# Optimization experiments

Measured on AMD Instinct MI355X. Metric: run time of the kernel, lower is better.

## Reference

```python
import jax, jax.numpy as jnp
import numpy as np

N, E, G, S = 200000, 800000, 2048, 128
NUM_OPS, NUM_ETYPES, NUMERIC = 64, 4, 12
H, TEXT, VOCAB, OUT = 256, 64, 30000, 512
IN0 = 32 + NUMERIC  # 44


def _ln(h, eps=1e-5):
    # nn.LayerNorm with default (ones/zeros) affine, created fresh each forward
    m = h.mean(-1, keepdims=True)
    v = ((h - m) ** 2).mean(-1, keepdims=True)
    return (h - m) * jax.lax.rsqrt(v + eps)


def _leaky(v):
    return jnp.where(v > 0, v, 0.1 * v)  # LeakyReLU(0.1)


def setup_inputs() -> dict:
    key = jax.random.key(0)
    ks = jax.random.split(key, 40)
    x = jax.random.normal(ks[0], (N, 1 + NUMERIC), jnp.float32)
    x = x.at[:, 0].set(jax.random.randint(ks[1], (N,), 0, NUM_OPS).astype(jnp.float32))
    inp = {
        'x': x,
        'edge_index': jax.random.randint(ks[2], (2, E), 0, N),
        'edge_attr': jax.random.randint(ks[3], (E,), 0, NUM_ETYPES),
        'batch': jnp.sort(jax.random.randint(ks[4], (N,), 0, G)),
        'sql_ids': jax.random.randint(ks[5], (G, S), 0, VOCAB),
        'sql_mask': (jax.random.uniform(ks[6], (G, S)) > 0.3).astype(jnp.float32),
        'op_embed': jax.random.normal(ks[7], (NUM_OPS, 32), jnp.float32),
        'edge_embed': jax.random.normal(ks[8], (NUM_ETYPES, 16), jnp.float32),
        'token_embed': jax.random.normal(ks[9], (VOCAB, TEXT), jnp.float32).at[0].set(0.0),  # padding_idx=0
    }
    dims = [IN0, H, H]
    k = 10
    for i, d in enumerate(dims):
        inp[f'lin_w{i}'] = jax.random.normal(ks[k], (d, 16), jnp.float32) * 0.05; k += 1
        inp[f'lin_b{i}'] = jnp.zeros((d,), jnp.float32)
        inp[f'eps{i}'] = jnp.zeros((), jnp.float32)  # train_eps init 0
        inp[f'W1_{i}'] = jax.random.normal(ks[k], (H, d), jnp.float32) * 0.05; k += 1
        inp[f'b1_{i}'] = jnp.zeros((H,), jnp.float32)
        inp[f'W2_{i}'] = jax.random.normal(ks[k], (H, H), jnp.float32) * 0.05; k += 1
        inp[f'b2_{i}'] = jnp.zeros((H,), jnp.float32)
    inp['mW1'] = jax.random.normal(ks[k], (H, H + 3 + TEXT), jnp.float32) * 0.05; k += 1
    inp['mb1'] = jnp.zeros((H,), jnp.float32)
    inp['mW2'] = jax.random.normal(ks[k], (OUT, H), jnp.float32) * 0.05
    inp['mb2'] = jnp.zeros((OUT,), jnp.float32)
    return inp


def reference(x, edge_index, edge_attr, batch, sql_ids, sql_mask,
              op_embed, edge_embed, token_embed,
              lin_w0, lin_b0, eps0, W1_0, b1_0, W2_0, b2_0,
              lin_w1, lin_b1, eps1, W1_1, b1_1, W2_1, b2_1,
              lin_w2, lin_b2, eps2, W1_2, b1_2, W2_2, b2_2,
              mW1, mb1, mW2, mb2):
    op_ids = jnp.clip(x[:, 0].astype(jnp.int32), 0, NUM_OPS - 1)
    nums = x[:, 1:]
    e_idx = jnp.minimum(edge_attr, NUM_ETYPES - 1)  # clamp_max
    edge_emb = edge_embed[e_idx]                    # [E,16]
    h = jnp.concatenate([op_embed[op_ids], nums], 1)  # [N,44]
    src, dst = edge_index[0], edge_index[1]
    convs = [(lin_w0, lin_b0, eps0, W1_0, b1_0, W2_0, b2_0),
             (lin_w1, lin_b1, eps1, W1_1, b1_1, W2_1, b2_1),
             (lin_w2, lin_b2, eps2, W1_2, b1_2, W2_2, b2_2)]
    for (lw, lb, eps, W1, b1, W2, b2) in convs:
        h_in = h
        # GINEConv: msg = relu(x_j + Lin(edge_attr)); sum-aggregate at dst
        msg = jax.nn.relu(h[src] + edge_emb @ lw.T + lb)        # [E,d]
        aggr = jax.ops.segment_sum(msg, dst, num_segments=h.shape[0])
        z = (1.0 + eps) * h + aggr
        h = jax.nn.relu(z @ W1.T + b1) @ W2.T + b2              # conv MLP -> [N,H]
        h = _ln(h)
        h = _leaky(h + h_in) if h_in.shape[-1] == h.shape[-1] else _leaky(h)
    # graph pooling
    g = jax.ops.segment_sum(h, batch, num_segments=G)            # global_add_pool
    count = jax.ops.segment_sum(jnp.ones((h.shape[0],), h.dtype), batch, num_segments=G)
    denom = jnp.maximum(count, 1.0)                              # scatter_mean semantics
    fanout_mean = jax.ops.segment_sum(x[:, 5], batch, num_segments=G) / denom
    cost_mean = jax.ops.segment_sum(x[:, 4], batch, num_segments=G) / denom
    graph_sum = jnp.stack([count, fanout_mean, cost_mean], 1)    # [G,3]
    # text pooling (masked mean)
    emb = token_embed[sql_ids]                                   # [G,S,TEXT]
    summed = (emb * sql_mask[..., None]).sum(1)
    lengths = jnp.maximum(sql_mask.sum(1, keepdims=True), 1.0)
    text_feat = summed / lengths
    cat = jnp.concatenate([g, graph_sum, text_feat], 1)          # [G, H+3+TEXT]
    hid = _leaky(cat @ mW1.T + mb1)                              # Dropout(0.1) is identity in eval
    return hid @ mW2.T + mb2                                     # [G, OUT]
```

## Files before the change

### kernel.cpp

```cpp
#include <hip/hip_runtime.h>

#define NN 200000
#define EE 800000
#define GG 2048
#define NBLK ((NN + 255) / 256)

typedef __attribute__((ext_vector_type(8))) short short8;
typedef __attribute__((ext_vector_type(4))) float f32x4;

__device__ __forceinline__ float bf2f(ushort u){
  unsigned x = ((unsigned)u) << 16;
  return __uint_as_float(x);
}
__device__ __forceinline__ ushort f2bf(float f){
  unsigned x = __float_as_uint(f);
  x += 0x7fffu + ((x >> 16) & 1u);
  return (ushort)(x >> 16);
}

__device__ __forceinline__ void swz256(const float* __restrict__ W, ushort* __restrict__ o, int idx){
  int ks = idx >> 13, rem = idx & 8191;
  int j16 = rem >> 9, rem2 = rem & 511;
  int ln = rem2 >> 3, t = rem2 & 7;
  int row = j16*16 + (ln & 15);
  int k = ks*32 + (ln >> 4)*8 + t;
  o[idx] = f2bf(W[(size_t)row*256 + k]);
}

__global__ __launch_bounds__(256) void prep_k(
    const float* __restrict__ W10, const float* __restrict__ W20,
    const float* __restrict__ W11, const float* __restrict__ W21,
    const float* __restrict__ W12, const float* __restrict__ W22,
    const float* __restrict__ lw0, const float* __restrict__ lb0,
    const float* __restrict__ lw1, const float* __restrict__ lb1,
    const float* __restrict__ lw2, const float* __restrict__ lb2,
    const float* __restrict__ eE, const float* __restrict__ mW1,
    const float* __restrict__ mW2,
    ushort* __restrict__ wb10, ushort* __restrict__ wb20,
    ushort* __restrict__ wb11, ushort* __restrict__ wb21,
    ushort* __restrict__ wb12, ushort* __restrict__ wb22,
    ushort* __restrict__ mW1b, ushort* __restrict__ mW2b,
    float* __restrict__ eb)
{
  int b = blockIdx.x, tid = threadIdx.x;
  if (b < 64){
    int idx = b*256 + tid;
    int ks = idx >> 13, rem = idx & 8191;
    int j16 = rem >> 9, rem2 = rem & 511;
    int ln = rem2 >> 3, t = rem2 & 7;
    int row = j16*16 + (ln & 15);
    int k = ks*32 + (ln >> 4)*8 + t;
    wb10[idx] = (k < 44) ? f2bf(W10[row*44 + k]) : (ushort)0;
    return;
  }
  b -= 64;
  if (b < 256){ swz256(W20, wb20, b*256+tid); return; } b -= 256;
  if (b < 256){ swz256(W11, wb11, b*256+tid); return; } b -= 256;
  if (b < 256){ swz256(W21, wb21, b*256+tid); return; } b -= 256;
  if (b < 256){ swz256(W12, wb12, b*256+tid); return; } b -= 256;
  if (b < 256){ swz256(W22, wb22, b*256+tid); return; } b -= 256;
  if (b < 384){
    int idx = b*256 + tid; int o = idx / 384, k = idx - o*384;
    mW1b[idx] = (k < 323) ? f2bf(mW1[(size_t)o*323 + k]) : (ushort)0;
    return;
  }
  b -= 384;
  if (b < 512){ int idx = b*256+tid; mW2b[idx] = f2bf(mW2[idx]); return; } b -= 512;
  int li = b >> 2, t = b & 3;
  const float* lw = (li == 0) ? lw0 : ((li == 1) ? lw1 : lw2);
  const float* lb = (li == 0) ? lb0 : ((li == 1) ? lb1 : lb2);
  int d = (li == 0) ? 44 : 256;
  float v = 0.f;
  if (tid < d){
    float a = 0.f;
    #pragma unroll
    for (int j = 0; j < 16; j++) a += eE[t*16 + j] * lw[tid*16 + j];
    v = a + lb[tid];
  }
  eb[(li*4 + t)*256 + tid] = v;
}

__global__ __launch_bounds__(256) void build_h0_k(
    const float* __restrict__ x, const float* __restrict__ opE, ushort* __restrict__ h0)
{
  int idx = blockIdx.x*256 + threadIdx.x;
  int i = idx >> 6, c = idx & 63;
  float v = 0.f;
  if (c < 32){
    int op = (int)x[(size_t)i*13];
    op = op < 0 ? 0 : (op > 63 ? 63 : op);
    v = opE[op*32 + c];
  } else if (c < 44){
    v = x[(size_t)i*13 + (c - 31)];
  }
  h0[idx] = f2bf(v);
}

__global__ __launch_bounds__(256) void deg_k(const int* __restrict__ dst, int* __restrict__ D){
  int e = blockIdx.x*256 + threadIdx.x;
  atomicAdd(&D[dst[e]], 1);
}
__global__ __launch_bounds__(256) void scan1_k(int* __restrict__ D, int* __restrict__ bsum){
  __shared__ int s[256];
  int b = blockIdx.x, t = threadIdx.x, idx = b*256 + t;
  int v = (idx < NN) ? D[idx] : 0;
  s[t] = v; __syncthreads();
  for (int off = 1; off < 256; off <<= 1){
    int u = (t >= off) ? s[t-off] : 0;
    __syncthreads();
    s[t] += u;
    __syncthreads();
  }
  if (idx < NN) D[idx] = s[t] - v;
  if (t == 255) bsum[b] = s[255];
}
__global__ __launch_bounds__(256) void scan2_k(int* __restrict__ bsum){
  __shared__ int s[256];
  __shared__ int carry;
  int t = threadIdx.x;
  if (t == 0) carry = 0;
  __syncthreads();
  for (int c0 = 0; c0 < NBLK; c0 += 256){
    int idx = c0 + t;
    int v = (idx < NBLK) ? bsum[idx] : 0;
    s[t] = v; __syncthreads();
    for (int off = 1; off < 256; off <<= 1){
      int u = (t >= off) ? s[t-off] : 0;
      __syncthreads();
      s[t] += u;
      __syncthreads();
    }
    int ex = s[t] - v + carry;
    if (idx < NBLK) bsum[idx] = ex;
    int tot = s[255];
    __syncthreads();
    if (t == 0) carry += tot;
    __syncthreads();
  }
}
__global__ __launch_bounds__(256) void scan3_k(int* __restrict__ D, const int* __restrict__ bsum){
  int b = blockIdx.x, idx = b*256 + threadIdx.x;
  if (idx < NN) D[idx] += bsum[b];
}
__global__ __launch_bounds__(256) void fill_k(const int* __restrict__ src, const int* __restrict__ dst,
                                              const int* __restrict__ et, int* __restrict__ D,
                                              int* __restrict__ csr){
  int e = blockIdx.x*256 + threadIdx.x;
  int d = dst[e];
  int t = et[e]; t = t < 3 ? t : 3;
  int pos = atomicAdd(&D[d], 1);
  csr[pos] = src[e] | (t << 18);
}

template<int KD, int RESID>
__global__ __launch_bounds__(256) void layerf_k(
    const ushort* __restrict__ hsrc, const int* __restrict__ Dend, const int* __restrict__ csr,
    const float* __restrict__ ebL,
    const ushort* __restrict__ W1s, const float* __restrict__ b1,
    const ushort* __restrict__ W2s, const float* __restrict__ b2,
    const float* __restrict__ epsp, ushort* __restrict__ hout)
{
  __shared__ ushort ZT[32][264];
  __shared__ float ebs[1024];
  __shared__ float red1[32][4], red2[32][4], mnL[32], rsL[32];
  const int tid = threadIdx.x, lane = tid & 63, wv = tid >> 6;
  const int l15 = lane & 15, lq = lane >> 4;
  const int rowBase = blockIdx.x * 32;
  const float epv = 1.0f + epsp[0];
  const char* hb = (const char*)hsrc;

  if (KD == 256){
    for (int i = tid; i < 1024; i += 256) ebs[i] = ebL[i];
  } else {
    if (tid < 256) ebs[tid] = ebL[(tid >> 6)*256 + (tid & 63)];
  }
  __syncthreads();

  if (KD == 256){
    const int c = lane * 4;
    const unsigned c2 = lane * 8;
    #pragma unroll 1
    for (int it = 0; it < 2; it++){
      int rr0 = wv*8 + it*4;
      int r0 = rowBase + rr0;
      float4 A0, A1, A2, A3;
      {
        ushort4 q0 = *(const ushort4*)(hb + (size_t)(r0+0)*512 + c2);
        ushort4 q1 = *(const ushort4*)(hb + (size_t)(r0+1)*512 + c2);
        ushort4 q2 = *(const ushort4*)(hb + (size_t)(r0+2)*512 + c2);
        ushort4 q3 = *(const ushort4*)(hb + (size_t)(r0+3)*512 + c2);
        A0 = make_float4(epv*bf2f(q0.x), epv*bf2f(q0.y), epv*bf2f(q0.z), epv*bf2f(q0.w));
        A1 = make_float4(epv*bf2f(q1.x), epv*bf2f(q1.y), epv*bf2f(q1.z), epv*bf2f(q1.w));
        A2 = make_float4(epv*bf2f(q2.x), epv*bf2f(q2.y), epv*bf2f(q2.z), epv*bf2f(q2.w));
        A3 = make_float4(epv*bf2f(q3.x), epv*bf2f(q3.y), epv*bf2f(q3.z), epv*bf2f(q3.w));
      }
      int bm1 = (r0 == 0) ? 0 : Dend[r0-1];
      int e0 = Dend[r0], e1 = Dend[r0+1], e2 = Dend[r0+2], e3 = Dend[r0+3];
      int st0 = bm1, st1 = e0, st2 = e1, st3 = e2;
      int n0 = e0 - st0, n1 = e1 - st1, n2 = e2 - st2, n3 = e3 - st3;
      int nmax = n0 > n1 ? n0 : n1;
      nmax = nmax > n2 ? nmax : n2;
      nmax = nmax > n3 ? nmax : n3;
      ushort4 z4; z4.x = z4.y = z4.z = z4.w = 0;
      ushort4 sv0 = z4, sv1 = z4, sv2 = z4, sv3 = z4;
      int t0 = 0, t1 = 0, t2 = 0, t3 = 0;
      if (n0 > 0){ int p = csr[st0]; sv0 = *(const ushort4*)(hb + (unsigned)((p & 0x3FFFF) << 9) + c2); t0 = ((p >> 18) & 3)*256; }
      if (n1 > 0){ int p = csr[st1]; sv1 = *(const ushort4*)(hb + (unsigned)((p & 0x3FFFF) << 9) + c2); t1 = ((p >> 18) & 3)*256; }
      if (n2 > 0){ int p = csr[st2]; sv2 = *(const ushort4*)(hb + (unsigned)((p & 0x3FFFF) << 9) + c2); t2 = ((p >> 18) & 3)*256; }
      if (n3 > 0){ int p = csr[st3]; sv3 = *(const ushort4*)(hb + (unsigned)((p & 0x3FFFF) << 9) + c2); t3 = ((p >> 18) & 3)*256; }
      for (int k = 0; k < nmax; k++){
        ushort4 c0 = sv0, c1 = sv1, c2v = sv2, c3 = sv3;
        int u0 = t0, u1 = t1, u2 = t2, u3 = t3;
        if (k+1 < n0){ int p = csr[st0+k+1]; sv0 = *(const ushort4*)(hb + (unsigned)((p & 0x3FFFF) << 9) + c2); t0 = ((p >> 18) & 3)*256; }
        if (k+1 < n1){ int p = csr[st1+k+1]; sv1 = *(const ushort4*)(hb + (unsigned)((p & 0x3FFFF) << 9) + c2); t1 = ((p >> 18) & 3)*256; }
        if (k+1 < n2){ int p = csr[st2+k+1]; sv2 = *(const ushort4*)(hb + (unsigned)((p & 0x3FFFF) << 9) + c2); t2 = ((p >> 18) & 3)*256; }
        if (k+1 < n3){ int p = csr[st3+k+1]; sv3 = *(const ushort4*)(hb + (unsigned)((p & 0x3FFFF) << 9) + c2); t3 = ((p >> 18) & 3)*256; }
        if (k < n0){
          const float4 ev = *(const float4*)&ebs[u0 + c];
          float v;
          v = bf2f(c0.x) + ev.x; A0.x += v > 0.f ? v : 0.f;
          v = bf2f(c0.y) + ev.y; A0.y += v > 0.f ? v : 0.f;
          v = bf2f(c0.z) + ev.z; A0.z += v > 0.f ? v : 0.f;
          v = bf2f(c0.w) + ev.w; A0.w += v > 0.f ? v : 0.f;
        }
        if (k < n1){
          const float4 ev = *(const float4*)&ebs[u1 + c];
          float v;
          v = bf2f(c1.x) + ev.x; A1.x += v > 0.f ? v : 0.f;
          v = bf2f(c1.y) + ev.y; A1.y += v > 0.f ? v : 0.f;
          v = bf2f(c1.z) + ev.z; A1.z += v > 0.f ? v : 0.f;
          v = bf2f(c1.w) + ev.w; A1.w += v > 0.f ? v : 0.f;
        }
        if (k < n2){
          const float4 ev = *(const float4*)&ebs[u2 + c];
          float v;
          v = bf2f(c2v.x) + ev.x; A2.x += v > 0.f ? v : 0.f;
          v = bf2f(c2v.y) + ev.y; A2.y += v > 0.f ? v : 0.f;
          v = bf2f(c2v.z) + ev.z; A2.z += v > 0.f ? v : 0.f;
          v = bf2f(c2v.w) + ev.w; A2.w += v > 0.f ? v : 0.f;
        }
        if (k < n3){
          const float4 ev = *(const float4*)&ebs[u3 + c];
          float v;
          v = bf2f(c3.x) + ev.x; A3.x += v > 0.f ? v : 0.f;
          v = bf2f(c3.y) + ev.y; A3.y += v > 0.f ? v : 0.f;
          v = bf2f(c3.z) + ev.z; A3.z += v > 0.f ? v : 0.f;
          v = bf2f(c3.w) + ev.w; A3.w += v > 0.f ? v : 0.f;
        }
      }
      ushort4 o;
      o.x = f2bf(A0.x); o.y = f2bf(A0.y); o.z = f2bf(A0.z); o.w = f2bf(A0.w);
      *(ushort4*)&ZT[rr0+0][c] = o;
      o.x = f2bf(A1.x); o.y = f2bf(A1.y); o.z = f2bf(A1.z); o.w = f2bf(A1.w);
      *(ushort4*)&ZT[rr0+1][c] = o;
      o.x = f2bf(A2.x); o.y = f2bf(A2.y); o.z = f2bf(A2.z); o.w = f2bf(A2.w);
      *(ushort4*)&ZT[rr0+2][c] = o;
      o.x = f2bf(A3.x); o.y = f2bf(A3.y); o.z = f2bf(A3.z); o.w = f2bf(A3.w);
      *(ushort4*)&ZT[rr0+3][c] = o;
    }
  } else {
    const int c = l15 * 4;
    const unsigned c2 = l15 * 8;
    #pragma unroll 1
    for (int it = 0; it < 2; it++){
      int rr = wv*8 + it*4 + lq;
      int r = rowBase + rr;
      const ushort4 hv = *(const ushort4*)(hb + (size_t)r*128 + c2);
      float a0 = epv*bf2f(hv.x), a1 = epv*bf2f(hv.y), a2 = epv*bf2f(hv.z), a3 = epv*bf2f(hv.w);
      int st = (r == 0) ? 0 : Dend[r-1];
      int en = Dend[r];
      if (st < en){
        int p = csr[st];
        ushort4 sv = *(const ushort4*)(hb + (unsigned)((p & 0x3FFFF) << 7) + c2);
        int tt = ((p >> 18) & 3)*64;
        for (int e = st; e < en; e++){
          ushort4 cur = sv; int tc = tt;
          int e2 = (e+1 < en) ? e+1 : e;
          int p2 = csr[e2];
          sv = *(const ushort4*)(hb + (unsigned)((p2 & 0x3FFFF) << 7) + c2);
          tt = ((p2 >> 18) & 3)*64;
          const float4 ev = *(const float4*)&ebs[tc + c];
          float v;
          v = bf2f(cur.x) + ev.x; a0 += v > 0.f ? v : 0.f;
          v = bf2f(cur.y) + ev.y; a1 += v > 0.f ? v : 0.f;
          v = bf2f(cur.z) + ev.z; a2 += v > 0.f ? v : 0.f;
          v = bf2f(cur.w) + ev.w; a3 += v > 0.f ? v : 0.f;
        }
      }
      ushort4 o; o.x=f2bf(a0); o.y=f2bf(a1); o.z=f2bf(a2); o.w=f2bf(a3);
      *(ushort4*)&ZT[rr][c] = o;
    }
  }
  __syncthreads();

  f32x4 acc[2][4];
  #pragma unroll
  for (int i = 0; i < 2; i++)
    #pragma unroll
    for (int j = 0; j < 4; j++){ f32x4 z = {0.f,0.f,0.f,0.f}; acc[i][j] = z; }

  #pragma unroll
  for (int s = 0; s < KD/32; s++){
    short8 af[2], bfv[4];
    #pragma unroll
    for (int j = 0; j < 4; j++)
      bfv[j] = *(const short8*)(W1s + ((size_t)(s*16 + wv*4 + j)*64 + lane)*8);
    #pragma unroll
    for (int i = 0; i < 2; i++)
      af[i] = *(const short8*)&ZT[i*16 + l15][s*32 + lq*8];
    #pragma unroll
    for (int i = 0; i < 2; i++)
      #pragma unroll
      for (int j = 0; j < 4; j++)
        acc[i][j] = __builtin_amdgcn_mfma_f32_16x16x32_bf16(af[i], bfv[j], acc[i][j], 0, 0, 0);
  }
  __syncthreads();

  {
    float b1c[4];
    #pragma unroll
    for (int j = 0; j < 4; j++) b1c[j] = b1[wv*64 + j*16 + l15];
    #pragma unroll
    for (int i = 0; i < 2; i++)
      #pragma unroll
      for (int j = 0; j < 4; j++){
        int cc = wv*64 + j*16 + l15;
        #pragma unroll
        for (int rg = 0; rg < 4; rg++){
          int r = i*16 + (lq << 2) + rg;
          float v = acc[i][j][rg] + b1c[j];
          v = v > 0.f ? v : 0.f;
          ZT[r][cc] = f2bf(v);
        }
      }
  }
  __syncthreads();

  #pragma unroll
  for (int i = 0; i < 2; i++)
    #pragma unroll
    for (int j = 0; j < 4; j++){ f32x4 z = {0.f,0.f,0.f,0.f}; acc[i][j] = z; }

  #pragma unroll
  for (int s = 0; s < 8; s++){
    short8 af[2], bfv[4];
    #pragma unroll
    for (int j = 0; j < 4; j++)
      bfv[j] = *(const short8*)(W2s + ((size_t)(s*16 + wv*4 + j)*64 + lane)*8);
    #pragma unroll
    for (int i = 0; i < 2; i++)
      af[i] = *(const short8*)&ZT[i*16 + l15][s*32 + lq*8];
    #pragma unroll
    for (int i = 0; i < 2; i++)
      #pragma unroll
      for (int j = 0; j < 4; j++)
        acc[i][j] = __builtin_amdgcn_mfma_f32_16x16x32_bf16(af[i], bfv[j], acc[i][j], 0, 0, 0);
  }

  float b2c[4];
  #pragma unroll
  for (int j = 0; j < 4; j++) b2c[j] = b2[wv*64 + j*16 + l15];
  #pragma unroll
  for (int i = 0; i < 2; i++){
    #pragma unroll
    for (int rg = 0; rg < 4; rg++){
      float s1 = 0.f, s2 = 0.f;
      #pragma unroll
      for (int j = 0; j < 4; j++){
        float y = acc[i][j][rg] + b2c[j];
        s1 += y; s2 += y*y;
      }
      #pragma unroll
      for (int m = 1; m < 16; m <<= 1){
        s1 += __shfl_xor(s1, m, 64);
        s2 += __shfl_xor(s2, m, 64);
      }
      if (l15 == 0){
        int r = i*16 + (lq << 2) + rg;
        red1[r][wv] = s1; red2[r][wv] = s2;
      }
    }
  }
  __syncthreads();
  if (tid < 32){
    float s1 = red1[tid][0] + red1[tid][1] + red1[tid][2] + red1[tid][3];
    float s2 = red2[tid][0] + red2[tid][1] + red2[tid][2] + red2[tid][3];
    float mn = s1 * (1.f/256.f);
    float vr = s2 * (1.f/256.f) - mn*mn;
    mnL[tid] = mn;
    rsL[tid] = rsqrtf(vr + 1e-5f);
  }
  __syncthreads();
  #pragma unroll
  for (int i = 0; i < 2; i++){
    #pragma unroll
    for (int rg = 0; rg < 4; rg++){
      int r = i*16 + (lq << 2) + rg;
      float mn = mnL[r], rs = rsL[r];
      #pragma unroll
      for (int j = 0; j < 4; j++){
        int cc = wv*64 + j*16 + l15;
        float y = acc[i][j][rg] + b2c[j];
        float v = (y - mn) * rs;
        if (RESID) v += bf2f(hsrc[(size_t)(rowBase + r)*256 + cc]);
        v = v > 0.f ? v : 0.1f*v;
        ZT[r][cc] = f2bf(v);
      }
    }
  }
  __syncthreads();
  #pragma unroll
  for (int p = 0; p < 8; p++){
    int r = p*4 + (tid >> 6);
    int c = (tid & 63) * 4;
    *(ushort4*)(hout + (size_t)(rowBase + r)*256 + c) = *(const ushort4*)&ZT[r][c];
  }
}

__global__ __launch_bounds__(256) void readout_k(
    const ushort* __restrict__ h, const int* __restrict__ batch, const float* __restrict__ x,
    const int* __restrict__ sqlIds, const float* __restrict__ sqlMask,
    const float* __restrict__ tok, ushort* __restrict__ catb)
{
  int g = blockIdx.x, tid = threadIdx.x;
  const int lane = tid & 63, wv = tid >> 6;
  __shared__ int se[2];
  __shared__ float part[4][256];
  __shared__ float tpart[4][64];
  __shared__ float mpart[4];
  __shared__ float xs[2];
  if (tid < 2){
    int target = g + tid;
    int lo = 0, hi = NN;
    while (lo < hi){ int mid = (lo + hi) >> 1; if (batch[mid] < target) lo = mid + 1; else hi = mid; }
    se[tid] = lo;
  }
  __syncthreads();
  int start = se[0], end = se[1];
  {
    float a0 = 0.f, a1 = 0.f, a2 = 0.f, a3 = 0.f;
    for (int i = start + wv; i < end; i += 4){
      ushort4 q = *(const ushort4*)(h + (size_t)i*256 + lane*4);
      a0 += bf2f(q.x); a1 += bf2f(q.y); a2 += bf2f(q.z); a3 += bf2f(q.w);
    }
    part[wv][lane*4 + 0] = a0;
    part[wv][lane*4 + 1] = a1;
    part[wv][lane*4 + 2] = a2;
    part[wv][lane*4 + 3] = a3;
  }
  if (wv >= 2){
    int col = (wv == 2) ? 5 : 4;
    float s = 0.f;
    for (int i = start + lane; i < end; i += 64) s += x[(size_t)i*13 + col];
    #pragma unroll
    for (int m = 1; m < 64; m <<= 1) s += __shfl_xor(s, m, 64);
    if (lane == 0) xs[wv - 2] = s;
  }
  {
    int c = lane;
    float acc = 0.f, m = 0.f;
    for (int s = wv; s < 128; s += 4){
      int id = sqlIds[g*128 + s];
      float mk = sqlMask[g*128 + s];
      m += mk;
      acc += tok[(size_t)id*64 + c] * mk;
    }
    tpart[wv][c] = acc;
    if (c == 0) mpart[wv] = m;
  }
  __syncthreads();
  {
    float gsum = part[0][tid] + part[1][tid] + part[2][tid] + part[3][tid];
    catb[(size_t)g*384 + tid] = f2bf(gsum);
  }
  if (tid == 0){
    float cnt = (float)(end - start);
    float dn = cnt > 1.f ? cnt : 1.f;
    catb[(size_t)g*384 + 256] = f2bf(cnt);
    catb[(size_t)g*384 + 257] = f2bf(xs[0] / dn);
    catb[(size_t)g*384 + 258] = f2bf(xs[1] / dn);
  }
  if (tid < 64){
    float L = mpart[0] + mpart[1] + mpart[2] + mpart[3];
    L = L > 1.f ? L : 1.f;
    float tsum = tpart[0][tid] + tpart[1][tid] + tpart[2][tid] + tpart[3][tid];
    catb[(size_t)g*384 + 259 + tid] = f2bf(tsum / L);
  }
  if (tid >= 64 && tid < 125){
    catb[(size_t)g*384 + 259 + tid] = 0;
  }
}

__global__ __launch_bounds__(256) void head1_k(
    const ushort* __restrict__ catb, const ushort* __restrict__ W1b,
    const float* __restrict__ b1, ushort* __restrict__ hidb)
{
  __shared__ ushort smem[64*72 + 256*72];
  ushort (*As)[72] = (ushort(*)[72])smem;
  ushort (*Ws)[72] = (ushort(*)[72])(smem + 64*72);
  const int tid = threadIdx.x, lane = tid & 63, wv = tid >> 6;
  const int rowBase = blockIdx.x * 64;
  f32x4 acc[4][4];
  #pragma unroll
  for (int i = 0; i < 4; i++)
    #pragma unroll
    for (int j = 0; j < 4; j++){ f32x4 z = {0.f,0.f,0.f,0.f}; acc[i][j] = z; }

  for (int k0 = 0; k0 < 384; k0 += 64){
    __syncthreads();
    #pragma unroll
    for (int p = 0; p < 4; p++){
      int r = p*16 + (tid >> 4);
      int kk = (tid & 15) * 4;
      *(ushort4*)&As[r][kk] = *(const ushort4*)(catb + (size_t)(rowBase + r)*384 + k0 + kk);
    }
    #pragma unroll
    for (int p = 0; p < 16; p++){
      int oc = p*16 + (tid >> 4);
      int kk = (tid & 15) * 4;
      *(ushort4*)&Ws[oc][kk] = *(const ushort4*)(W1b + (size_t)oc*384 + k0 + kk);
    }
    __syncthreads();
    #pragma unroll
    for (int kc = 0; kc < 2; kc++){
      short8 af[4], bfv[4];
      #pragma unroll
      for (int i = 0; i < 4; i++)
        af[i] = *(const short8*)&As[i*16 + (lane & 15)][kc*32 + (lane >> 4)*8];
      #pragma unroll
      for (int j = 0; j < 4; j++)
        bfv[j] = *(const short8*)&Ws[wv*64 + j*16 + (lane & 15)][kc*32 + (lane >> 4)*8];
      #pragma unroll
      for (int i = 0; i < 4; i++)
        #pragma unroll
        for (int j = 0; j < 4; j++)
          acc[i][j] = __builtin_amdgcn_mfma_f32_16x16x32_bf16(af[i], bfv[j], acc[i][j], 0, 0, 0);
    }
  }
  __syncthreads();
  ushort (*Cs)[264] = (ushort(*)[264])smem;
  #pragma unroll
  for (int j = 0; j < 4; j++){
    int cc = wv*64 + j*16 + (lane & 15);
    float bb = b1[cc];
    #pragma unroll
    for (int i = 0; i < 4; i++){
      #pragma unroll
      for (int rg = 0; rg < 4; rg++){
        int r = i*16 + ((lane >> 4) << 2) + rg;
        float v = acc[i][j][rg] + bb;
        v = v > 0.f ? v : 0.1f*v;
        Cs[r][cc] = f2bf(v);
      }
    }
  }
  __syncthreads();
  #pragma unroll
  for (int p = 0; p < 16; p++){
    int r = p*4 + (tid >> 6);
    int c = (tid & 63) * 4;
    *(ushort4*)(hidb + (size_t)(rowBase + r)*256 + c) = *(const ushort4*)&Cs[r][c];
  }
}

__global__ __launch_bounds__(256) void head2_k(
    const ushort* __restrict__ hidb, const ushort* __restrict__ W2b,
    const float* __restrict__ b2, float* __restrict__ out)
{
  __shared__ float smemf[128*132];
  ushort (*As)[72] = (ushort(*)[72])smemf;
  ushort (*Bs)[72] = (ushort(*)[72])((ushort*)smemf + 128*72);
  const int tid = threadIdx.x, lane = tid & 63, wv = tid >> 6;
  const int wr = (wv >> 1) * 64;
  const int wc = (wv & 1) * 64;
  const int rowBase = blockIdx.x * 128;
  const int colBase = blockIdx.y * 128;
  const int lr = tid >> 4, lk = (tid & 15) * 4;

  f32x4 acc[4][4];
  #pragma unroll
  for (int i = 0; i < 4; i++)
    #pragma unroll
    for (int j = 0; j < 4; j++){ f32x4 z = {0.f,0.f,0.f,0.f}; acc[i][j] = z; }

  for (int k0 = 0; k0 < 256; k0 += 64){
    __syncthreads();
    #pragma unroll
    for (int p = 0; p < 8; p++){
      int r = lr + p*16;
      *(ushort4*)&As[r][lk] = *(const ushort4*)(hidb + (size_t)(rowBase + r)*256 + k0 + lk);
      *(ushort4*)&Bs[r][lk] = *(const ushort4*)(W2b + (size_t)(colBase + r)*256 + k0 + lk);
    }
    __syncthreads();
    #pragma unroll
    for (int kc = 0; kc < 2; kc++){
      short8 af[4], bfv[4];
      #pragma unroll
      for (int i = 0; i < 4; i++)
        af[i] = *(const short8*)&As[wr + i*16 + (lane & 15)][kc*32 + (lane >> 4)*8];
      #pragma unroll
      for (int j = 0; j < 4; j++)
        bfv[j] = *(const short8*)&Bs[wc + j*16 + (lane & 15)][kc*32 + (lane >> 4)*8];
      #pragma unroll
      for (int i = 0; i < 4; i++)
        #pragma unroll
        for (int j = 0; j < 4; j++)
          acc[i][j] = __builtin_amdgcn_mfma_f32_16x16x32_bf16(af[i], bfv[j], acc[i][j], 0, 0, 0);
    }
  }
  __syncthreads();
  float (*Cs)[132] = (float(*)[132])smemf;
  #pragma unroll
  for (int j = 0; j < 4; j++){
    int cl = wc + j*16 + (lane & 15);
    float bb = b2[colBase + cl];
    #pragma unroll
    for (int i = 0; i < 4; i++){
      int r0 = wr + i*16 + ((lane >> 4) << 2);
      #pragma unroll
      for (int rg = 0; rg < 4; rg++)
        Cs[r0 + rg][cl] = acc[i][j][rg] + bb;
    }
  }
  __syncthreads();
  #pragma unroll
  for (int p = 0; p < 16; p++){
    int r = (tid >> 5) + p*8;
    int c4 = (tid & 31) * 4;
    *(float4*)(out + (size_t)(rowBase + r)*512 + colBase + c4) = *(const float4*)&Cs[r][c4];
  }
}

extern "C" void kernel_launch(void* const* d_in, const int* in_sizes, int n_in,
                              void* d_out, int out_size, void* d_ws, size_t ws_size,
                              hipStream_t stream)
{
  const float* x       = (const float*)d_in[0];
  const int*   ei      = (const int*)d_in[1];
  const int*   src     = ei;
  const int*   dst     = ei + EE;
  const int*   eattr   = (const int*)d_in[2];
  const int*   batch   = (const int*)d_in[3];
  const int*   sqlIds  = (const int*)d_in[4];
  const float* sqlMask = (const float*)d_in[5];
  const float* opE     = (const float*)d_in[6];
  const float* eE      = (const float*)d_in[7];
  const float* tok     = (const float*)d_in[8];
  const float* lw0 = (const float*)d_in[9],  *lb0 = (const float*)d_in[10], *eps0 = (const float*)d_in[11];
  const float* W10 = (const float*)d_in[12], *b10 = (const float*)d_in[13];
  const float* W20 = (const float*)d_in[14], *b20 = (const float*)d_in[15];
  const float* lw1 = (const float*)d_in[16], *lb1 = (const float*)d_in[17], *eps1 = (const float*)d_in[18];
  const float* W11 = (const float*)d_in[19], *b11 = (const float*)d_in[20];
  const float* W21 = (const float*)d_in[21], *b21 = (const float*)d_in[22];
  const float* lw2 = (const float*)d_in[23], *lb2 = (const float*)d_in[24], *eps2 = (const float*)d_in[25];
  const float* W12 = (const float*)d_in[26], *b12 = (const float*)d_in[27];
  const float* W22 = (const float*)d_in[28], *b22 = (const float*)d_in[29];
  const float* mW1 = (const float*)d_in[30], *mb1 = (const float*)d_in[31];
  const float* mW2 = (const float*)d_in[32], *mb2 = (const float*)d_in[33];
  float* out = (float*)d_out;

  char* ws = (char*)d_ws;
  size_t off = 0;
  const size_t NB256 = (size_t)NN*256*2;
  ushort* bufH    = (ushort*)(ws + off); off += NB256;
  char*   region  = ws + off;            off += NB256;
  ushort* h0      = (ushort*)region;
  ushort* hPong   = (ushort*)region;
  ushort* catb    = (ushort*)region;
  ushort* hidb    = (ushort*)(region + (size_t)GG*384*2);
  ushort* wb10 = (ushort*)(ws + off); off += (size_t)256*64*2;
  ushort* wb20 = (ushort*)(ws + off); off += (size_t)65536*2;
  ushort* wb11 = (ushort*)(ws + off); off += (size_t)65536*2;
  ushort* wb21 = (ushort*)(ws + off); off += (size_t)65536*2;
  ushort* wb12 = (ushort*)(ws + off); off += (size_t)65536*2;
  ushort* wb22 = (ushort*)(ws + off); off += (size_t)65536*2;
  ushort* mW1b = (ushort*)(ws + off); off += (size_t)256*384*2;
  ushort* mW2b = (ushort*)(ws + off); off += (size_t)512*256*2;
  float*  eb   = (float*)(ws + off);  off += (size_t)3*4*256*4;
  int* D    = (int*)(ws + off); off += (size_t)NN*4;
  int* bsum = (int*)(ws + off); off += (size_t)NBLK*4;
  int* csr  = (int*)(ws + off); off += (size_t)EE*4;
  size_t needFast = off;

  if (ws_size < needFast) return;

  prep_k<<<2252, 256, 0, stream>>>(W10, W20, W11, W21, W12, W22,
                                   lw0, lb0, lw1, lb1, lw2, lb2, eE, mW1, mW2,
                                   wb10, wb20, wb11, wb21, wb12, wb22, mW1b, mW2b, eb);
  build_h0_k<<<50000, 256, 0, stream>>>(x, opE, h0);

  hipMemsetAsync(D, 0, (size_t)NN*4, stream);
  deg_k<<<3125, 256, 0, stream>>>(dst, D);
  scan1_k<<<NBLK, 256, 0, stream>>>(D, bsum);
  scan2_k<<<1, 256, 0, stream>>>(bsum);
  scan3_k<<<NBLK, 256, 0, stream>>>(D, bsum);
  fill_k<<<3125, 256, 0, stream>>>(src, dst, eattr, D, csr);

  layerf_k<64,0><<<6250, 256, 0, stream>>>(h0,    D, csr, eb,        wb10, b10, wb20, b20, eps0, bufH);
  layerf_k<256,1><<<6250, 256, 0, stream>>>(bufH, D, csr, eb + 1024, wb11, b11, wb21, b21, eps1, hPong);
  layerf_k<256,1><<<6250, 256, 0, stream>>>(hPong,D, csr, eb + 2048, wb12, b12, wb22, b22, eps2, bufH);

  readout_k<<<GG, 256, 0, stream>>>(bufH, batch, x, sqlIds, sqlMask, tok, catb);
  head1_k<<<32, 256, 0, stream>>>(catb, mW1b, mb1, hidb);
  head2_k<<<dim3(16, 4), 256, 0, stream>>>(hidb, mW2b, mb2, out);
}
```

Before: 840.3 us.

## Gather 8 rows per wave with deeper CSR prefetch and coalesced residual add

The KD=256 aggregation now has each wave process all 8 of its rows in one pass instead of two passes of 4. The CSR index is prefetched two edges ahead, so more independent gather loads are in flight to hide memory latency. The KD=64 path likewise handles two rows per lane together. The residual add and LeakyReLU move to the final write-out stage, where the residual is read with coalesced ushort4 loads instead of scalar strided loads. This adds an extra bf16 rounding before the residual add and raises register pressure.

Result: slower. 903.4 us (+7.5%).

```diff
diff --git a/kernel.cpp b/kernel.cpp
--- a/kernel.cpp
+++ b/kernel.cpp
@@ -179,117 +179,125 @@
   if (KD == 256){
     const int c = lane * 4;
     const unsigned c2 = lane * 8;
-    #pragma unroll 1
-    for (int it = 0; it < 2; it++){
-      int rr0 = wv*8 + it*4;
-      int r0 = rowBase + rr0;
-      float4 A0, A1, A2, A3;
-      {
-        ushort4 q0 = *(const ushort4*)(hb + (size_t)(r0+0)*512 + c2);
-        ushort4 q1 = *(const ushort4*)(hb + (size_t)(r0+1)*512 + c2);
-        ushort4 q2 = *(const ushort4*)(hb + (size_t)(r0+2)*512 + c2);
-        ushort4 q3 = *(const ushort4*)(hb + (size_t)(r0+3)*512 + c2);
-        A0 = make_float4(epv*bf2f(q0.x), epv*bf2f(q0.y), epv*bf2f(q0.z), epv*bf2f(q0.w));
-        A1 = make_float4(epv*bf2f(q1.x), epv*bf2f(q1.y), epv*bf2f(q1.z), epv*bf2f(q1.w));
-        A2 = make_float4(epv*bf2f(q2.x), epv*bf2f(q2.y), epv*bf2f(q2.z), epv*bf2f(q2.w));
-        A3 = make_float4(epv*bf2f(q3.x), epv*bf2f(q3.y), epv*bf2f(q3.z), epv*bf2f(q3.w));
-      }
-      int bm1 = (r0 == 0) ? 0 : Dend[r0-1];
-      int e0 = Dend[r0], e1 = Dend[r0+1], e2 = Dend[r0+2], e3 = Dend[r0+3];
-      int st0 = bm1, st1 = e0, st2 = e1, st3 = e2;
-      int n0 = e0 - st0, n1 = e1 - st1, n2 = e2 - st2, n3 = e3 - st3;
-      int nmax = n0 > n1 ? n0 : n1;
-      nmax = nmax > n2 ? nmax : n2;
-      nmax = nmax > n3 ? nmax : n3;
-      ushort4 z4; z4.x = z4.y = z4.z = z4.w = 0;
-      ushort4 sv0 = z4, sv1 = z4, sv2 = z4, sv3 = z4;
-      int t0 = 0, t1 = 0, t2 = 0, t3 = 0;
-      if (n0 > 0){ int p = csr[st0]; sv0 = *(const ushort4*)(hb + (unsigned)((p & 0x3FFFF) << 9) + c2); t0 = ((p >> 18) & 3)*256; }
-      if (n1 > 0){ int p = csr[st1]; sv1 = *(const ushort4*)(hb + (unsigned)((p & 0x3FFFF) << 9) + c2); t1 = ((p >> 18) & 3)*256; }
-      if (n2 > 0){ int p = csr[st2]; sv2 = *(const ushort4*)(hb + (unsigned)((p & 0x3FFFF) << 9) + c2); t2 = ((p >> 18) & 3)*256; }
-      if (n3 > 0){ int p = csr[st3]; sv3 = *(const ushort4*)(hb + (unsigned)((p & 0x3FFFF) << 9) + c2); t3 = ((p >> 18) & 3)*256; }
-      for (int k = 0; k < nmax; k++){
-        ushort4 c0 = sv0, c1 = sv1, c2v = sv2, c3 = sv3;
-        int u0 = t0, u1 = t1, u2 = t2, u3 = t3;
-        if (k+1 < n0){ int p = csr[st0+k+1]; sv0 = *(const ushort4*)(hb + (unsigned)((p & 0x3FFFF) << 9) + c2); t0 = ((p >> 18) & 3)*256; }
-        if (k+1 < n1){ int p = csr[st1+k+1]; sv1 = *(const ushort4*)(hb + (unsigned)((p & 0x3FFFF) << 9) + c2); t1 = ((p >> 18) & 3)*256; }
-        if (k+1 < n2){ int p = csr[st2+k+1]; sv2 = *(const ushort4*)(hb + (unsigned)((p & 0x3FFFF) << 9) + c2); t2 = ((p >> 18) & 3)*256; }
-        if (k+1 < n3){ int p = csr[st3+k+1]; sv3 = *(const ushort4*)(hb + (unsigned)((p & 0x3FFFF) << 9) + c2); t3 = ((p >> 18) & 3)*256; }
-        if (k < n0){
-          const float4 ev = *(const float4*)&ebs[u0 + c];
+    const int r0 = rowBase + wv*8;
+    float4 A[8];
+    #pragma unroll
+    for (int j = 0; j < 8; j++){
+      ushort4 q = *(const ushort4*)(hb + (size_t)(r0+j)*512 + c2);
+      A[j] = make_float4(epv*bf2f(q.x), epv*bf2f(q.y), epv*bf2f(q.z), epv*bf2f(q.w));
+    }
+    int st[8], nn[8];
+    {
+      int prev = (r0 == 0) ? 0 : Dend[r0-1];
+      #pragma unroll
+      for (int j = 0; j < 8; j++){
+        int e = Dend[r0+j];
+        st[j] = prev; nn[j] = e - prev; prev = e;
+      }
+    }
+    int nmax = 0;
+    #pragma unroll
+    for (int j = 0; j < 8; j++) nmax = nn[j] > nmax ? nn[j] : nmax;
+
+    ushort4 sv[8]; int tt[8]; int p1[8];
+    #pragma unroll
+    for (int j = 0; j < 8; j++){
+      sv[j].x = sv[j].y = sv[j].z = sv[j].w = 0; tt[j] = 0; p1[j] = 0;
+      if (nn[j] > 0){
+        int p = csr[st[j]];
+        sv[j] = *(const ushort4*)(hb + (unsigned)((p & 0x3FFFF) << 9) + c2);
+        tt[j] = ((p >> 18) & 3)*256;
+      }
+    }
+    #pragma unroll
+    for (int j = 0; j < 8; j++)
+      if (nn[j] > 1) p1[j] = csr[st[j]+1];
+
+    for (int k = 0; k < nmax; k++){
+      #pragma unroll
+      for (int j = 0; j < 8; j++){
+        if (k < nn[j]){
+          ushort4 cu = sv[j];
+          const float4 ev = *(const float4*)&ebs[tt[j] + c];
+          if (k+1 < nn[j]){
+            int p = p1[j];
+            sv[j] = *(const ushort4*)(hb + (unsigned)((p & 0x3FFFF) << 9) + c2);
+            tt[j] = ((p >> 18) & 3)*256;
+            if (k+2 < nn[j]) p1[j] = csr[st[j]+k+2];
+          }
           float v;
-          v = bf2f(c0.x) + ev.x; A0.x += v > 0.f ? v : 0.f;
-          v = bf2f(c0.y) + ev.y; A0.y += v > 0.f ? v : 0.f;
-          v = bf2f(c0.z) + ev.z; A0.z += v > 0.f ? v : 0.f;
-          v = bf2f(c0.w) + ev.w; A0.w += v > 0.f ? v : 0.f;
+          v = bf2f(cu.x) + ev.x; A[j].x += v > 0.f ? v : 0.f;
+          v = bf2f(cu.y) + ev.y; A[j].y += v > 0.f ? v : 0.f;
+          v = bf2f(cu.z) + ev.z; A[j].z += v > 0.f ? v : 0.f;
+          v = bf2f(cu.w) + ev.w; A[j].w += v > 0.f ? v : 0.f;
         }
-        if (k < n1){
-          const float4 ev = *(const float4*)&ebs[u1 + c];
-          float v;
-          v = bf2f(c1.x) + ev.x; A1.x += v > 0.f ? v : 0.f;
-          v = bf2f(c1.y) + ev.y; A1.y += v > 0.f ? v : 0.f;
-          v = bf2f(c1.z) + ev.z; A1.z += v > 0.f ? v : 0.f;
-          v = bf2f(c1.w) + ev.w; A1.w += v > 0.f ? v : 0.f;
-        }
-        if (k < n2){
-          const float4 ev = *(const float4*)&ebs[u2 + c];
-          float v;
-          v = bf2f(c2v.x) + ev.x; A2.x += v > 0.f ? v : 0.f;
-          v = bf2f(c2v.y) + ev.y; A2.y += v > 0.f ? v : 0.f;
-          v = bf2f(c2v.z) + ev.z; A2.z += v > 0.f ? v : 0.f;
-          v = bf2f(c2v.w) + ev.w; A2.w += v > 0.f ? v : 0.f;
-        }
-        if (k < n3){
-          const float4 ev = *(const float4*)&ebs[u3 + c];
-          float v;
-          v = bf2f(c3.x) + ev.x; A3.x += v > 0.f ? v : 0.f;
-          v = bf2f(c3.y) + ev.y; A3.y += v > 0.f ? v : 0.f;
-          v = bf2f(c3.z) + ev.z; A3.z += v > 0.f ? v : 0.f;
-          v = bf2f(c3.w) + ev.w; A3.w += v > 0.f ? v : 0.f;
-        }
-      }
+      }
+    }
+    #pragma unroll
+    for (int j = 0; j < 8; j++){
       ushort4 o;
-      o.x = f2bf(A0.x); o.y = f2bf(A0.y); o.z = f2bf(A0.z); o.w = f2bf(A0.w);
-      *(ushort4*)&ZT[rr0+0][c] = o;
-      o.x = f2bf(A1.x); o.y = f2bf(A1.y); o.z = f2bf(A1.z); o.w = f2bf(A1.w);
-      *(ushort4*)&ZT[rr0+1][c] = o;
-      o.x = f2bf(A2.x); o.y = f2bf(A2.y); o.z = f2bf(A2.z); o.w = f2bf(A2.w);
-      *(ushort4*)&ZT[rr0+2][c] = o;
-      o.x = f2bf(A3.x); o.y = f2bf(A3.y); o.z = f2bf(A3.z); o.w = f2bf(A3.w);
-      *(ushort4*)&ZT[rr0+3][c] = o;
+      o.x = f2bf(A[j].x); o.y = f2bf(A[j].y); o.z = f2bf(A[j].z); o.w = f2bf(A[j].w);
+      *(ushort4*)&ZT[wv*8 + j][c] = o;
     }
   } else {
     const int c = l15 * 4;
     const unsigned c2 = l15 * 8;
-    #pragma unroll 1
-    for (int it = 0; it < 2; it++){
-      int rr = wv*8 + it*4 + lq;
-      int r = rowBase + rr;
-      const ushort4 hv = *(const ushort4*)(hb + (size_t)r*128 + c2);
-      float a0 = epv*bf2f(hv.x), a1 = epv*bf2f(hv.y), a2 = epv*bf2f(hv.z), a3 = epv*bf2f(hv.w);
-      int st = (r == 0) ? 0 : Dend[r-1];
-      int en = Dend[r];
-      if (st < en){
-        int p = csr[st];
-        ushort4 sv = *(const ushort4*)(hb + (unsigned)((p & 0x3FFFF) << 7) + c2);
-        int tt = ((p >> 18) & 3)*64;
-        for (int e = st; e < en; e++){
-          ushort4 cur = sv; int tc = tt;
-          int e2 = (e+1 < en) ? e+1 : e;
-          int p2 = csr[e2];
-          sv = *(const ushort4*)(hb + (unsigned)((p2 & 0x3FFFF) << 7) + c2);
-          tt = ((p2 >> 18) & 3)*64;
-          const float4 ev = *(const float4*)&ebs[tc + c];
-          float v;
-          v = bf2f(cur.x) + ev.x; a0 += v > 0.f ? v : 0.f;
-          v = bf2f(cur.y) + ev.y; a1 += v > 0.f ? v : 0.f;
-          v = bf2f(cur.z) + ev.z; a2 += v > 0.f ? v : 0.f;
-          v = bf2f(cur.w) + ev.w; a3 += v > 0.f ? v : 0.f;
+    const int rrA = wv*8 + lq, rrB = rrA + 4;
+    const int rA = rowBase + rrA, rB = rowBase + rrB;
+    float aA0, aA1, aA2, aA3, aB0, aB1, aB2, aB3;
+    {
+      ushort4 hv = *(const ushort4*)(hb + (size_t)rA*128 + c2);
+      aA0 = epv*bf2f(hv.x); aA1 = epv*bf2f(hv.y); aA2 = epv*bf2f(hv.z); aA3 = epv*bf2f(hv.w);
+      hv = *(const ushort4*)(hb + (size_t)rB*128 + c2);
+      aB0 = epv*bf2f(hv.x); aB1 = epv*bf2f(hv.y); aB2 = epv*bf2f(hv.z); aB3 = epv*bf2f(hv.w);
+    }
+    int stA = (rA == 0) ? 0 : Dend[rA-1], enA = Dend[rA];
+    int stB = Dend[rB-1], enB = Dend[rB];
+    int nA = enA - stA, nB = enB - stB;
+    int nmax = nA > nB ? nA : nB;
+    ushort4 svA, svB; int ttA = 0, ttB = 0, pA = 0, pB = 0;
+    svA.x = svA.y = svA.z = svA.w = 0; svB = svA;
+    if (nA > 0){ int p = csr[stA]; svA = *(const ushort4*)(hb + (unsigned)((p & 0x3FFFF) << 7) + c2); ttA = ((p >> 18) & 3)*64; }
+    if (nB > 0){ int p = csr[stB]; svB = *(const ushort4*)(hb + (unsigned)((p & 0x3FFFF) << 7) + c2); ttB = ((p >> 18) & 3)*64; }
+    if (nA > 1) pA = csr[stA+1];
+    if (nB > 1) pB = csr[stB+1];
+    for (int k = 0; k < nmax; k++){
+      if (k < nA){
+        ushort4 cu = svA;
+        const float4 ev = *(const float4*)&ebs[ttA + c];
+        if (k+1 < nA){
+          int p = pA;
+          svA = *(const ushort4*)(hb + (unsigned)((p & 0x3FFFF) << 7) + c2);
+          ttA = ((p >> 18) & 3)*64;
+          if (k+2 < nA) pA = csr[stA+k+2];
         }
-      }
-      ushort4 o; o.x=f2bf(a0); o.y=f2bf(a1); o.z=f2bf(a2); o.w=f2bf(a3);
-      *(ushort4*)&ZT[rr][c] = o;
-    }
+        float v;
+        v = bf2f(cu.x) + ev.x; aA0 += v > 0.f ? v : 0.f;
+        v = bf2f(cu.y) + ev.y; aA1 += v > 0.f ? v : 0.f;
+        v = bf2f(cu.z) + ev.z; aA2 += v > 0.f ? v : 0.f;
+        v = bf2f(cu.w) + ev.w; aA3 += v > 0.f ? v : 0.f;
+      }
+      if (k < nB){
+        ushort4 cu = svB;
+        const float4 ev = *(const float4*)&ebs[ttB + c];
+        if (k+1 < nB){
+          int p = pB;
+          svB = *(const ushort4*)(hb + (unsigned)((p & 0x3FFFF) << 7) + c2);
+          ttB = ((p >> 18) & 3)*64;
+          if (k+2 < nB) pB = csr[stB+k+2];
+        }
+        float v;
+        v = bf2f(cu.x) + ev.x; aB0 += v > 0.f ? v : 0.f;
+        v = bf2f(cu.y) + ev.y; aB1 += v > 0.f ? v : 0.f;
+        v = bf2f(cu.z) + ev.z; aB2 += v > 0.f ? v : 0.f;
+        v = bf2f(cu.w) + ev.w; aB3 += v > 0.f ? v : 0.f;
+      }
+    }
+    ushort4 o;
+    o.x = f2bf(aA0); o.y = f2bf(aA1); o.z = f2bf(aA2); o.w = f2bf(aA3);
+    *(ushort4*)&ZT[rrA][c] = o;
+    o.x = f2bf(aB0); o.y = f2bf(aB1); o.z = f2bf(aB2); o.w = f2bf(aB3);
+    *(ushort4*)&ZT[rrB][c] = o;
   }
   __syncthreads();
 
@@ -402,18 +410,40 @@
         int cc = wv*64 + j*16 + l15;
         float y = acc[i][j][rg] + b2c[j];
         float v = (y - mn) * rs;
-        if (RESID) v += bf2f(hsrc[(size_t)(rowBase + r)*256 + cc]);
-        v = v > 0.f ? v : 0.1f*v;
+        if (!RESID) v = v > 0.f ? v : 0.1f*v;
         ZT[r][cc] = f2bf(v);
       }
+    }
+  }
+  ushort4 res[8];
+  if (RESID){
+    #pragma unroll
+    for (int p = 0; p < 8; p++){
+      int r = p*4 + (tid >> 6);
+      int cs = (tid & 63) * 4;
+      res[p] = *(const ushort4*)(hsrc + (size_t)(rowBase + r)*256 + cs);
     }
   }
   __syncthreads();
   #pragma unroll
   for (int p = 0; p < 8; p++){
     int r = p*4 + (tid >> 6);
-    int c = (tid & 63) * 4;
-    *(ushort4*)(hout + (size_t)(rowBase + r)*256 + c) = *(const ushort4*)&ZT[r][c];
+    int cs = (tid & 63) * 4;
+    ushort4 zt = *(const ushort4*)&ZT[r][cs];
+    ushort4 o;
+    if (RESID){
+      float v0 = bf2f(zt.x) + bf2f(res[p].x);
+      float v1 = bf2f(zt.y) + bf2f(res[p].y);
+      float v2 = bf2f(zt.z) + bf2f(res[p].z);
+      float v3 = bf2f(zt.w) + bf2f(res[p].w);
+      o.x = f2bf(v0 > 0.f ? v0 : 0.1f*v0);
+      o.y = f2bf(v1 > 0.f ? v1 : 0.1f*v1);
+      o.z = f2bf(v2 > 0.f ? v2 : 0.1f*v2);
+      o.w = f2bf(v3 > 0.f ? v3 : 0.1f*v3);
+    } else {
+      o = zt;
+    }
+    *(ushort4*)(hout + (size_t)(rowBase + r)*256 + cs) = o;
   }
 }
 
```

## Deepen CSR index prefetch, interleave two rows in small gather, coalesce residual add

Applied to the files above, without the earlier changes.

In the KD=256 gather, the CSR entry for the next-next edge is now prefetched a step ahead, so each neighbour row load no longer waits on a dependent index load. An opaque zero register keeps the compiler from hoisting or merging these loads. The KD=64 path processes its two rows together in one loop with the same two-deep prefetch, giving more independent memory requests in flight. The residual add and LeakyReLU move from a scattered per-element read into the final coalesced ushort4 store loop. The residual is now added after the LN output is rounded to bf16, which changes rounding slightly, and the extra live registers may lower occupancy.

Measured after the change: 831.2 us. Within noise of the previous version (-1.1%).

```diff
diff --git a/kernel.cpp b/kernel.cpp
--- a/kernel.cpp
+++ b/kernel.cpp
@@ -177,6 +177,7 @@
   __syncthreads();
 
   if (KD == 256){
+    int nz; asm("v_mov_b32 %0, 0" : "=v"(nz));
     const int c = lane * 4;
     const unsigned c2 = lane * 8;
     #pragma unroll 1
@@ -204,17 +205,22 @@
       ushort4 z4; z4.x = z4.y = z4.z = z4.w = 0;
       ushort4 sv0 = z4, sv1 = z4, sv2 = z4, sv3 = z4;
       int t0 = 0, t1 = 0, t2 = 0, t3 = 0;
-      if (n0 > 0){ int p = csr[st0]; sv0 = *(const ushort4*)(hb + (unsigned)((p & 0x3FFFF) << 9) + c2); t0 = ((p >> 18) & 3)*256; }
-      if (n1 > 0){ int p = csr[st1]; sv1 = *(const ushort4*)(hb + (unsigned)((p & 0x3FFFF) << 9) + c2); t1 = ((p >> 18) & 3)*256; }
-      if (n2 > 0){ int p = csr[st2]; sv2 = *(const ushort4*)(hb + (unsigned)((p & 0x3FFFF) << 9) + c2); t2 = ((p >> 18) & 3)*256; }
-      if (n3 > 0){ int p = csr[st3]; sv3 = *(const ushort4*)(hb + (unsigned)((p & 0x3FFFF) << 9) + c2); t3 = ((p >> 18) & 3)*256; }
+      int q0 = 0, q1 = 0, q2 = 0, q3 = 0;
+      if (n0 > 0){ int p = csr[st0 + nz]; sv0 = *(const ushort4*)(hb + (unsigned)((p & 0x3FFFF) << 9) + c2); t0 = ((p >> 18) & 3)*256; }
+      if (n1 > 0){ int p = csr[st1 + nz]; sv1 = *(const ushort4*)(hb + (unsigned)((p & 0x3FFFF) << 9) + c2); t1 = ((p >> 18) & 3)*256; }
+      if (n2 > 0){ int p = csr[st2 + nz]; sv2 = *(const ushort4*)(hb + (unsigned)((p & 0x3FFFF) << 9) + c2); t2 = ((p >> 18) & 3)*256; }
+      if (n3 > 0){ int p = csr[st3 + nz]; sv3 = *(const ushort4*)(hb + (unsigned)((p & 0x3FFFF) << 9) + c2); t3 = ((p >> 18) & 3)*256; }
+      if (n0 > 1) q0 = csr[st0 + 1 + nz];
+      if (n1 > 1) q1 = csr[st1 + 1 + nz];
+      if (n2 > 1) q2 = csr[st2 + 1 + nz];
+      if (n3 > 1) q3 = csr[st3 + 1 + nz];
       for (int k = 0; k < nmax; k++){
         ushort4 c0 = sv0, c1 = sv1, c2v = sv2, c3 = sv3;
         int u0 = t0, u1 = t1, u2 = t2, u3 = t3;
-        if (k+1 < n0){ int p = csr[st0+k+1]; sv0 = *(const ushort4*)(hb + (unsigned)((p & 0x3FFFF) << 9) + c2); t0 = ((p >> 18) & 3)*256; }
-        if (k+1 < n1){ int p = csr[st1+k+1]; sv1 = *(const ushort4*)(hb + (unsigned)((p & 0x3FFFF) << 9) + c2); t1 = ((p >> 18) & 3)*256; }
-        if (k+1 < n2){ int p = csr[st2+k+1]; sv2 = *(const ushort4*)(hb + (unsigned)((p & 0x3FFFF) << 9) + c2); t2 = ((p >> 18) & 3)*256; }
-        if (k+1 < n3){ int p = csr[st3+k+1]; sv3 = *(const ushort4*)(hb + (unsigned)((p & 0x3FFFF) << 9) + c2); t3 = ((p >> 18) & 3)*256; }
+        if (k+1 < n0){ int p = q0; sv0 = *(const ushort4*)(hb + (unsigned)((p & 0x3FFFF) << 9) + c2); t0 = ((p >> 18) & 3)*256; if (k+2 < n0) q0 = csr[st0 + k + 2 + nz]; }
+        if (k+1 < n1){ int p = q1; sv1 = *(const ushort4*)(hb + (unsigned)((p & 0x3FFFF) << 9) + c2); t1 = ((p >> 18) & 3)*256; if (k+2 < n1) q1 = csr[st1 + k + 2 + nz]; }
+        if (k+1 < n2){ int p = q2; sv2 = *(const ushort4*)(hb + (unsigned)((p & 0x3FFFF) << 9) + c2); t2 = ((p >> 18) & 3)*256; if (k+2 < n2) q2 = csr[st2 + k + 2 + nz]; }
+        if (k+1 < n3){ int p = q3; sv3 = *(const ushort4*)(hb + (unsigned)((p & 0x3FFFF) << 9) + c2); t3 = ((p >> 18) & 3)*256; if (k+2 < n3) q3 = csr[st3 + k + 2 + nz]; }
         if (k < n0){
           const float4 ev = *(const float4*)&ebs[u0 + c];
           float v;
@@ -261,35 +267,62 @@
   } else {
     const int c = l15 * 4;
     const unsigned c2 = l15 * 8;
-    #pragma unroll 1
-    for (int it = 0; it < 2; it++){
-      int rr = wv*8 + it*4 + lq;
-      int r = rowBase + rr;
-      const ushort4 hv = *(const ushort4*)(hb + (size_t)r*128 + c2);
-      float a0 = epv*bf2f(hv.x), a1 = epv*bf2f(hv.y), a2 = epv*bf2f(hv.z), a3 = epv*bf2f(hv.w);
-      int st = (r == 0) ? 0 : Dend[r-1];
-      int en = Dend[r];
-      if (st < en){
-        int p = csr[st];
-        ushort4 sv = *(const ushort4*)(hb + (unsigned)((p & 0x3FFFF) << 7) + c2);
-        int tt = ((p >> 18) & 3)*64;
-        for (int e = st; e < en; e++){
-          ushort4 cur = sv; int tc = tt;
-          int e2 = (e+1 < en) ? e+1 : e;
-          int p2 = csr[e2];
-          sv = *(const ushort4*)(hb + (unsigned)((p2 & 0x3FFFF) << 7) + c2);
-          tt = ((p2 >> 18) & 3)*64;
-          const float4 ev = *(const float4*)&ebs[tc + c];
-          float v;
-          v = bf2f(cur.x) + ev.x; a0 += v > 0.f ? v : 0.f;
-          v = bf2f(cur.y) + ev.y; a1 += v > 0.f ? v : 0.f;
-          v = bf2f(cur.z) + ev.z; a2 += v > 0.f ? v : 0.f;
-          v = bf2f(cur.w) + ev.w; a3 += v > 0.f ? v : 0.f;
+    const int rrA = wv*8 + lq, rrB = rrA + 4;
+    const int rA = rowBase + rrA, rB = rowBase + rrB;
+    float aA0, aA1, aA2, aA3, aB0, aB1, aB2, aB3;
+    {
+      ushort4 hv = *(const ushort4*)(hb + (size_t)rA*128 + c2);
+      aA0 = epv*bf2f(hv.x); aA1 = epv*bf2f(hv.y); aA2 = epv*bf2f(hv.z); aA3 = epv*bf2f(hv.w);
+      hv = *(const ushort4*)(hb + (size_t)rB*128 + c2);
+      aB0 = epv*bf2f(hv.x); aB1 = epv*bf2f(hv.y); aB2 = epv*bf2f(hv.z); aB3 = epv*bf2f(hv.w);
+    }
+    int stA = (rA == 0) ? 0 : Dend[rA-1], enA = Dend[rA];
+    int stB = Dend[rB-1], enB = Dend[rB];
+    int nA = enA - stA, nB = enB - stB;
+    int nmax = nA > nB ? nA : nB;
+    ushort4 svA, svB; int ttA = 0, ttB = 0, pA = 0, pB = 0;
+    svA.x = svA.y = svA.z = svA.w = 0; svB = svA;
+    if (nA > 0){ int p = csr[stA]; svA = *(const ushort4*)(hb + (unsigned)((p & 0x3FFFF) << 7) + c2); ttA = ((p >> 18) & 3)*64; }
+    if (nB > 0){ int p = csr[stB]; svB = *(const ushort4*)(hb + (unsigned)((p & 0x3FFFF) << 7) + c2); ttB = ((p >> 18) & 3)*64; }
+    if (nA > 1) pA = csr[stA+1];
+    if (nB > 1) pB = csr[stB+1];
+    for (int k = 0; k < nmax; k++){
+      if (k < nA){
+        ushort4 cu = svA;
+        const float4 ev = *(const float4*)&ebs[ttA + c];
+        if (k+1 < nA){
+          int p = pA;
+          svA = *(const ushort4*)(hb + (unsigned)((p & 0x3FFFF) << 7) + c2);
+          ttA = ((p >> 18) & 3)*64;
+          if (k+2 < nA) pA = csr[stA+k+2];
         }
-      }
-      ushort4 o; o.x=f2bf(a0); o.y=f2bf(a1); o.z=f2bf(a2); o.w=f2bf(a3);
-      *(ushort4*)&ZT[rr][c] = o;
-    }
+        float v;
+        v = bf2f(cu.x) + ev.x; aA0 += v > 0.f ? v : 0.f;
+        v = bf2f(cu.y) + ev.y; aA1 += v > 0.f ? v : 0.f;
+        v = bf2f(cu.z) + ev.z; aA2 += v > 0.f ? v : 0.f;
+        v = bf2f(cu.w) + ev.w; aA3 += v > 0.f ? v : 0.f;
+      }
+      if (k < nB){
+        ushort4 cu = svB;
+        const float4 ev = *(const float4*)&ebs[ttB + c];
+        if (k+1 < nB){
+          int p = pB;
+          svB = *(const ushort4*)(hb + (unsigned)((p & 0x3FFFF) << 7) + c2);
+          ttB = ((p >> 18) & 3)*64;
+          if (k+2 < nB) pB = csr[stB+k+2];
+        }
+        float v;
+        v = bf2f(cu.x) + ev.x; aB0 += v > 0.f ? v : 0.f;
+        v = bf2f(cu.y) + ev.y; aB1 += v > 0.f ? v : 0.f;
+        v = bf2f(cu.z) + ev.z; aB2 += v > 0.f ? v : 0.f;
+        v = bf2f(cu.w) + ev.w; aB3 += v > 0.f ? v : 0.f;
+      }
+    }
+    ushort4 o;
+    o.x = f2bf(aA0); o.y = f2bf(aA1); o.z = f2bf(aA2); o.w = f2bf(aA3);
+    *(ushort4*)&ZT[rrA][c] = o;
+    o.x = f2bf(aB0); o.y = f2bf(aB1); o.z = f2bf(aB2); o.w = f2bf(aB3);
+    *(ushort4*)&ZT[rrB][c] = o;
   }
   __syncthreads();
 
@@ -402,8 +435,7 @@
         int cc = wv*64 + j*16 + l15;
         float y = acc[i][j][rg] + b2c[j];
         float v = (y - mn) * rs;
-        if (RESID) v += bf2f(hsrc[(size_t)(rowBase + r)*256 + cc]);
-        v = v > 0.f ? v : 0.1f*v;
+        if (!RESID) v = v > 0.f ? v : 0.1f*v;
         ZT[r][cc] = f2bf(v);
       }
     }
@@ -412,8 +444,23 @@
   #pragma unroll
   for (int p = 0; p < 8; p++){
     int r = p*4 + (tid >> 6);
-    int c = (tid & 63) * 4;
-    *(ushort4*)(hout + (size_t)(rowBase + r)*256 + c) = *(const ushort4*)&ZT[r][c];
+    int cs = (tid & 63) * 4;
+    ushort4 zt = *(const ushort4*)&ZT[r][cs];
+    ushort4 o;
+    if (RESID){
+      ushort4 rv = *(const ushort4*)(hsrc + (size_t)(rowBase + r)*256 + cs);
+      float v0 = bf2f(zt.x) + bf2f(rv.x);
+      float v1 = bf2f(zt.y) + bf2f(rv.y);
+      float v2 = bf2f(zt.z) + bf2f(rv.z);
+      float v3 = bf2f(zt.w) + bf2f(rv.w);
+      o.x = f2bf(v0 > 0.f ? v0 : 0.1f*v0);
+      o.y = f2bf(v1 > 0.f ? v1 : 0.1f*v1);
+      o.z = f2bf(v2 > 0.f ? v2 : 0.1f*v2);
+      o.w = f2bf(v3 > 0.f ? v3 : 0.1f*v3);
+    } else {
+      o = zt;
+    }
+    *(ushort4*)(hout + (size_t)(rowBase + r)*256 + cs) = o;
   }
 }
 
```
